# Performance work log

Measured on AMD Instinct MI355X. Metric: run time of the kernel, lower is better.

## Reference

```python
import jax, jax.numpy as jnp
import numpy as np


def setup_inputs() -> dict:
    key = jax.random.key(0)
    ks = jax.random.split(key, 6)
    B, La, Lb = 32, 2048, 2048
    return {
        "a": jax.random.normal(ks[0], (B, La), dtype=jnp.float32),
        "b": jax.random.normal(ks[1], (B, Lb), dtype=jnp.float32),
        "in_proj_w": jax.random.normal(ks[2], (3, 1), dtype=jnp.float32),
        "in_proj_b": jax.random.normal(ks[3], (3,), dtype=jnp.float32) * 0.1,
        "out_w": jax.random.normal(ks[4], (1, 1), dtype=jnp.float32),
        "out_b": jax.random.normal(ks[5], (1,), dtype=jnp.float32) * 0.1,
    }


def reference(a, b, in_proj_w, in_proj_b, out_w, out_b):
    # embed_dim=1, num_heads=1 MHA degenerates to scalar affine projections.
    wq, wk, wv = in_proj_w[0, 0], in_proj_w[1, 0], in_proj_w[2, 0]
    bq, bk, bv = in_proj_b[0], in_proj_b[1], in_proj_b[2]
    q = a * wq + bq                      # [B, La]
    k = b * wk + bk                      # [B, Lb]
    v = b * wv + bv                      # [B, Lb]
    # scale = 1/sqrt(head_dim=1) = 1; scores via outer product per batch
    scores = q[:, :, None] * k[:, None, :]        # [B, La, Lb]
    attn = jax.nn.softmax(scores, axis=-1)        # [B, La, Lb]
    ctx = jnp.einsum("bqk,bk->bq", attn, v)       # [B, La]
    x = ctx * out_w[0, 0] + out_b[0]              # out_proj (1x1)
    # residual with a_f, then exact (erf) GELU as in F.gelu default
    return jax.nn.gelu(x + a, approximate=False)[..., None]  # [B, La, 1]
```

## Files before the change

kernel.cpp:

```cpp
#include <hip/hip_runtime.h>
#include <math.h>


#define BATCH 32
#define LA 2048
#define LB 2048
#define SPLIT 8
#define MI 4
#define CHUNK (LB / SPLIT)
#define CPAD (CHUNK + 1)
#define THREADS 256
#define I_PER_BLOCK (THREADS / SPLIT * MI)
#define BLOCKS_PER_B (LA / I_PER_BLOCK)

__global__ __launch_bounds__(THREADS, 2)
void cross_attn_kernel(const float* __restrict__ a,
                       const float* __restrict__ b,
                       const float* __restrict__ w_in,
                       const float* __restrict__ b_in,
                       const float* __restrict__ w_out,
                       const float* __restrict__ b_out,
                       float* __restrict__ out)
{
    __shared__ float k_lds[SPLIT * CPAD];
    __shared__ float v_lds[SPLIT * CPAD];
    __shared__ float red[8];

    const int tid = threadIdx.x;
    const int bb  = blockIdx.x / BLOCKS_PER_B;
    const int cc  = blockIdx.x % BLOCKS_PER_B;

    const float wq = w_in[0], wk = w_in[1], wv = w_in[2];
    const float bq = b_in[0], bk = b_in[1], bv = b_in[2];
    const float ow = w_out[0], ob = b_out[0];

    const float* brow = b + (size_t)bb * LB;
    float kmaxl = -INFINITY, kminl = INFINITY;
    {
        const int j0 = tid * 8;
        float4 b0 = *(const float4*)(brow + j0);
        float4 b1 = *(const float4*)(brow + j0 + 4);
        float bvals[8] = {b0.x, b0.y, b0.z, b0.w, b1.x, b1.y, b1.z, b1.w};
        const int base = (j0 >> 8) * CPAD + (j0 & (CHUNK - 1));
        #pragma unroll
        for (int e = 0; e < 8; ++e) {
            float kj = fmaf(bvals[e], wk, bk);
            float vj = fmaf(bvals[e], wv, bv);
            k_lds[base + e] = kj;
            v_lds[base + e] = vj;
            kmaxl = fmaxf(kmaxl, kj);
            kminl = fminf(kminl, kj);
        }
    }

    #pragma unroll
    for (int off = 1; off < 64; off <<= 1) {
        kmaxl = fmaxf(kmaxl, __shfl_xor(kmaxl, off, 64));
        kminl = fminf(kminl, __shfl_xor(kminl, off, 64));
    }
    const int lane = tid & 63, wave = tid >> 6;
    if (lane == 0) { red[wave] = kmaxl; red[4 + wave] = kminl; }
    __syncthreads();
    const float kmax = fmaxf(fmaxf(red[0], red[1]), fmaxf(red[2], red[3]));
    const float kmin = fminf(fminf(red[4], red[5]), fminf(red[6], red[7]));

    const int split = tid & (SPLIT - 1);
    const int oct   = tid >> 3;
    const int i0    = cc * I_PER_BLOCK + oct * MI;
    const float4 av = *(const float4*)(a + (size_t)bb * LA + i0);
    const float avals[MI] = {av.x, av.y, av.z, av.w};

    const float L2E = 1.4426950408889634f;
    float t2[MI], m2[MI], num[MI], den[MI];
    #pragma unroll
    for (int m = 0; m < MI; ++m) {
        float t = fmaf(avals[m], wq, bq);
        t2[m] = t * L2E;
        m2[m] = (t2[m] >= 0.0f) ? t2[m] * kmax : t2[m] * kmin;
        num[m] = 0.0f;
        den[m] = 0.0f;
    }

    const float* kp = k_lds + split * CPAD;
    const float* vp = v_lds + split * CPAD;

    #pragma unroll 4
    for (int jj = 0; jj < CHUNK; ++jj) {
        const float kk = kp[jj];
        const float vv = vp[jj];
        #pragma unroll
        for (int m = 0; m < MI; ++m) {
            float e = __builtin_amdgcn_exp2f(fmaf(t2[m], kk, -m2[m]));
            num[m] = fmaf(e, vv, num[m]);
            den[m] += e;
        }
    }

    #pragma unroll
    for (int mask = 1; mask < SPLIT; mask <<= 1) {
        #pragma unroll
        for (int m = 0; m < MI; ++m) {
            num[m] += __shfl_xor(num[m], mask, 64);
            den[m] += __shfl_xor(den[m], mask, 64);
        }
    }

    if (split == 0) {
        float4 res;
        float* rp = &res.x;
        #pragma unroll
        for (int m = 0; m < MI; ++m) {
            float ctx = num[m] / den[m];
            float x   = fmaf(ctx, ow, ob);
            float y   = x + avals[m];
            rp[m] = 0.5f * y * (1.0f + erff(y * 0.70710678118654752f));
        }
        *(float4*)(out + (size_t)bb * LA + i0) = res;
    }
}

extern "C" void kernel_launch(void* const* d_in, const int* in_sizes, int n_in,
                              void* d_out, int out_size, void* d_ws, size_t ws_size,
                              hipStream_t stream) {
    const float* a  = (const float*)d_in[0];
    const float* b  = (const float*)d_in[1];
    const float* wi = (const float*)d_in[2];
    const float* bi = (const float*)d_in[3];
    const float* wo = (const float*)d_in[4];
    const float* bo = (const float*)d_in[5];
    float* out = (float*)d_out;

    dim3 grid(BATCH * BLOCKS_PER_B);
    dim3 block(THREADS);
    cross_attn_kernel<<<grid, block, 0, stream>>>(a, b, wi, bi, wo, bo, out);
}
```

Baseline: 85.05 us.

## Interleave K/V into float4 LDS pairs and double key split per query

K and V are now stored interleaved in shared memory as float4 {k0,v0,k1,v1}, so each thread fetches two keys with a single 128-bit LDS read instead of two scalar reads per key. The key split doubles from 8 to 16, which halves the queries per block and doubles the block count, and the launch bounds request 4 blocks per CU. The aim is to cut LDS instruction count and raise occupancy and latency hiding, at the cost of more blocks each recomputing K/V and the max/min reduction, plus an extra shuffle-reduction stage.

```diff
diff --git a/kernel.cpp b/kernel.cpp
--- a/kernel.cpp
+++ b/kernel.cpp
@@ -5,15 +5,16 @@
 #define BATCH 32
 #define LA 2048
 #define LB 2048
-#define SPLIT 8
+#define SPLIT 16
 #define MI 4
 #define CHUNK (LB / SPLIT)
-#define CPAD (CHUNK + 1)
+#define P2 (CHUNK / 2)
+#define CP (P2 + 1)
 #define THREADS 256
-#define I_PER_BLOCK (THREADS / SPLIT * MI)
-#define BLOCKS_PER_B (LA / I_PER_BLOCK)
+#define IPB ((THREADS / SPLIT) * MI)
+#define BLOCKS_PER_B (LA / IPB)
 
-__global__ __launch_bounds__(THREADS, 2)
+__global__ __launch_bounds__(THREADS, 4)
 void cross_attn_kernel(const float* __restrict__ a,
                        const float* __restrict__ b,
                        const float* __restrict__ w_in,
@@ -22,8 +23,7 @@
                        const float* __restrict__ b_out,
                        float* __restrict__ out)
 {
-    __shared__ float k_lds[SPLIT * CPAD];
-    __shared__ float v_lds[SPLIT * CPAD];
+    __shared__ float4 kv[SPLIT * CP];
     __shared__ float red[8];
 
     const int tid = threadIdx.x;
@@ -40,16 +40,19 @@
         const int j0 = tid * 8;
         float4 b0 = *(const float4*)(brow + j0);
         float4 b1 = *(const float4*)(brow + j0 + 4);
-        float bvals[8] = {b0.x, b0.y, b0.z, b0.w, b1.x, b1.y, b1.z, b1.w};
-        const int base = (j0 >> 8) * CPAD + (j0 & (CHUNK - 1));
+        float bv8[8] = {b0.x, b0.y, b0.z, b0.w, b1.x, b1.y, b1.z, b1.w};
+        const int c  = j0 >> 7;
+        const int pi = (j0 & (CHUNK - 1)) >> 1;
+        float4* dst = &kv[c * CP + pi];
         #pragma unroll
-        for (int e = 0; e < 8; ++e) {
-            float kj = fmaf(bvals[e], wk, bk);
-            float vj = fmaf(bvals[e], wv, bv);
-            k_lds[base + e] = kj;
-            v_lds[base + e] = vj;
-            kmaxl = fmaxf(kmaxl, kj);
-            kminl = fminf(kminl, kj);
+        for (int e = 0; e < 4; ++e) {
+            float k0 = fmaf(bv8[2 * e],     wk, bk);
+            float v0 = fmaf(bv8[2 * e],     wv, bv);
+            float k1 = fmaf(bv8[2 * e + 1], wk, bk);
+            float v1 = fmaf(bv8[2 * e + 1], wv, bv);
+            dst[e] = make_float4(k0, v0, k1, v1);
+            kmaxl = fmaxf(kmaxl, fmaxf(k0, k1));
+            kminl = fminf(kminl, fminf(k0, k1));
         }
     }
 
@@ -65,34 +68,35 @@
     const float kmin = fminf(fminf(red[4], red[5]), fminf(red[6], red[7]));
 
     const int split = tid & (SPLIT - 1);
-    const int oct   = tid >> 3;
-    const int i0    = cc * I_PER_BLOCK + oct * MI;
+    const int g     = tid >> 4;
+    const int i0    = cc * IPB + g * MI;
     const float4 av = *(const float4*)(a + (size_t)bb * LA + i0);
     const float avals[MI] = {av.x, av.y, av.z, av.w};
 
     const float L2E = 1.4426950408889634f;
-    float t2[MI], m2[MI], num[MI], den[MI];
+    float t2[MI], nm2[MI], num[MI], den[MI];
     #pragma unroll
     for (int m = 0; m < MI; ++m) {
         float t = fmaf(avals[m], wq, bq);
-        t2[m] = t * L2E;
-        m2[m] = (t2[m] >= 0.0f) ? t2[m] * kmax : t2[m] * kmin;
+        t2[m]  = t * L2E;
+        nm2[m] = -((t2[m] >= 0.0f) ? t2[m] * kmax : t2[m] * kmin);
         num[m] = 0.0f;
         den[m] = 0.0f;
     }
 
-    const float* kp = k_lds + split * CPAD;
-    const float* vp = v_lds + split * CPAD;
+    const float4* kvp = &kv[split * CP];
 
-    #pragma unroll 4
-    for (int jj = 0; jj < CHUNK; ++jj) {
-        const float kk = kp[jj];
-        const float vv = vp[jj];
+    #pragma unroll 8
+    for (int p = 0; p < P2; ++p) {
+        const float4 q = kvp[p];
         #pragma unroll
         for (int m = 0; m < MI; ++m) {
-            float e = __builtin_amdgcn_exp2f(fmaf(t2[m], kk, -m2[m]));
-            num[m] = fmaf(e, vv, num[m]);
-            den[m] += e;
+            float e0 = __builtin_amdgcn_exp2f(fmaf(t2[m], q.x, nm2[m]));
+            num[m] = fmaf(e0, q.y, num[m]);
+            den[m] += e0;
+            float e1 = __builtin_amdgcn_exp2f(fmaf(t2[m], q.z, nm2[m]));
+            num[m] = fmaf(e1, q.w, num[m]);
+            den[m] += e1;
         }
     }
 
```

Result: no change. 83.96 us (-1.3%).
